# Kernel tuning notes

Measured on AMD Instinct MI355X. Metric: run time of the kernel, lower is better.

The kernel has to match this reference:

```python
import jax, jax.numpy as jnp
import numpy as np

D_MODEL = 1024
N_TILES = 16
N_CLASSES = 1024
BATCH = 65536
THRESH = 0.3  # ternary quantization threshold


def setup_inputs() -> dict:
    key = jax.random.key(0)
    k_x, k_s, k_w, k_b = jax.random.split(key, 4)
    x = jax.random.normal(k_x, (BATCH, D_MODEL), dtype=jnp.float32)
    # signatures_raw: n_tiles params of shape [d_model], init randn*0.5
    sigs_raw = jax.random.normal(k_s, (N_TILES, D_MODEL), dtype=jnp.float32) * 0.5
    # per-tile Linear(d_model, n_classes): weight [n_classes, d_model], bias [n_classes]
    lim = 1.0 / np.sqrt(D_MODEL)
    W = jax.random.uniform(k_w, (N_TILES, N_CLASSES, D_MODEL), dtype=jnp.float32, minval=-lim, maxval=lim)
    b = jax.random.uniform(k_b, (N_TILES, N_CLASSES), dtype=jnp.float32, minval=-lim, maxval=lim)
    return {"x": x, "sigs_raw": sigs_raw, "W": W, "b": b}


def _quantize_ternary(s):
    # straight-through ternary: forward = {-1, 0, +1}, backward = identity
    q = jnp.where(s > THRESH, 1.0, jnp.where(s < -THRESH, -1.0, 0.0)).astype(s.dtype)
    return s + jax.lax.stop_gradient(q - s)


def reference(x, sigs_raw, W, b):
    sigs = _quantize_ternary(sigs_raw)           # [T, D]
    scores = x @ sigs.T                          # [B, T]
    tile_indices = jnp.argmax(scores, axis=-1)   # [B]
    n_tiles = W.shape[0]
    logits = jnp.zeros((x.shape[0], W.shape[1]), dtype=x.dtype)  # [B, C]
    # fixed small loop over tiles (experts); select per-token result via mask
    for t in range(n_tiles):
        out_t = x @ W[t].T + b[t]                # [B, C]
        logits = jnp.where((tile_indices == t)[:, None], out_t, logits)
    return logits, tile_indices
```

## Files before the change

kernel.cpp:

```cpp
#include <hip/hip_runtime.h>
#include <hip/hip_bf16.h>
#include <stdint.h>

#define B_TOK 65536
#define DM 1024
#define NC 1024
#define NT 16
#define GAPTHR 0.25f

typedef __attribute__((ext_vector_type(4))) float f32x4;
typedef __attribute__((ext_vector_type(4))) unsigned int u32x4;
typedef __attribute__((ext_vector_type(2))) unsigned int u32x2;
typedef __attribute__((ext_vector_type(4))) unsigned short u16x4;
typedef __attribute__((ext_vector_type(8))) short short8;

#define AS1(p) ((__attribute__((address_space(1))) void*)(p))
#define AS3(p) ((__attribute__((address_space(3))) void*)(p))

static __device__ inline unsigned short f2bf(float f) {
  __hip_bfloat16 h = __float2bfloat16(f);
  unsigned short u;
  __builtin_memcpy(&u, &h, 2);
  return u;
}
#define PK8(a, b, old, w) __builtin_amdgcn_cvt_pk_fp8_f32((a), (b), (old), (w))

__global__ void k_prep(const float* __restrict__ sigs, unsigned int* __restrict__ mask,
                       unsigned short* __restrict__ Sb) {
  int d = threadIdx.x;
  unsigned int m = 0;
#pragma unroll
  for (int t = 0; t < NT; ++t) {
    float s = sigs[t * DM + d];
    float q = (s > 0.3f) ? 1.0f : ((s < -0.3f) ? -1.0f : 0.0f);
    if (s > 0.3f) m |= 1u << t;
    else if (s < -0.3f) m |= 1u << (16 + t);
    Sb[t * DM + d] = f2bf(q);
  }
  mask[d] = m;
}

__global__ __launch_bounds__(256) void k_pre(const float* __restrict__ x,
    const unsigned short* __restrict__ Sb, unsigned char* __restrict__ xb,
    int* __restrict__ tidx, float* __restrict__ oidx,
    int* __restrict__ fixlist, int* __restrict__ nfix, int* __restrict__ counts,
    const float* __restrict__ W, unsigned char* __restrict__ Wb)
{
  int bid = blockIdx.x;
  int tid = threadIdx.x;
  if (bid >= 1024) {
    const f32x4* W4 = (const f32x4*)W;
    unsigned int* O = (unsigned int*)Wb;
    int n4 = NT * NC * DM / 4;
    for (int i = (bid - 1024) * 256 + tid; i < n4; i += 512 * 256) {
      f32x4 v = W4[i];
      unsigned int p = PK8(v[0] * 16.f, v[1] * 16.f, 0, 0);
      p = PK8(v[2] * 16.f, v[3] * 16.f, p, 1);
      O[i] = p;
    }
    return;
  }
  __shared__ int hist[16];
  if (tid < 16) hist[tid] = 0;
  __syncthreads();

  int w = tid >> 6, l = tid & 63;
  int lr = l & 15, lg = l >> 4;
  int tok0 = bid * 64 + w * 16;

  const float* xr = x + (size_t)(tok0 + lr) * DM + lg * 8;
  unsigned char* xbr = xb + (size_t)(tok0 + lr) * DM + lg * 8;
  const unsigned short* sr = Sb + (size_t)lr * DM + lg * 8;

  f32x4 accA = (f32x4){0.f, 0.f, 0.f, 0.f};
  f32x4 accB = (f32x4){0.f, 0.f, 0.f, 0.f};
  for (int kc = 0; kc < 32; kc += 2) {
    f32x4 v0 = *(const f32x4*)(xr + kc * 32);
    f32x4 v1 = *(const f32x4*)(xr + kc * 32 + 4);
    f32x4 v2 = *(const f32x4*)(xr + kc * 32 + 32);
    f32x4 v3 = *(const f32x4*)(xr + kc * 32 + 36);
    short8 a0, a1;
#pragma unroll
    for (int j = 0; j < 4; ++j) {
      a0[j]     = (short)f2bf(v0[j]);
      a0[4 + j] = (short)f2bf(v1[j]);
      a1[j]     = (short)f2bf(v2[j]);
      a1[4 + j] = (short)f2bf(v3[j]);
    }
    u32x2 p0, p1;
    p0[0] = PK8(v0[0], v0[1], 0, 0); p0[0] = PK8(v0[2], v0[3], p0[0], 1);
    p0[1] = PK8(v1[0], v1[1], 0, 0); p0[1] = PK8(v1[2], v1[3], p0[1], 1);
    p1[0] = PK8(v2[0], v2[1], 0, 0); p1[0] = PK8(v2[2], v2[3], p1[0], 1);
    p1[1] = PK8(v3[0], v3[1], 0, 0); p1[1] = PK8(v3[2], v3[3], p1[1], 1);
    *(u32x2*)(xbr + kc * 32) = p0;
    *(u32x2*)(xbr + kc * 32 + 32) = p1;
    short8 b0 = *(const short8*)(sr + kc * 32);
    short8 b1 = *(const short8*)(sr + kc * 32 + 32);
    accA = __builtin_amdgcn_mfma_f32_16x16x32_bf16(a0, b0, accA, 0, 0, 0);
    accB = __builtin_amdgcn_mfma_f32_16x16x32_bf16(a1, b1, accB, 0, 0, 0);
  }
  f32x4 acc;
#pragma unroll
  for (int i = 0; i < 4; ++i) acc[i] = accA[i] + accB[i];

  float m1[4], m2v[4]; int i1[4];
#pragma unroll
  for (int i = 0; i < 4; ++i) { m1[i] = acc[i]; i1[i] = lr; m2v[i] = -1e30f; }
#pragma unroll
  for (int off = 1; off < 16; off <<= 1) {
#pragma unroll
    for (int i = 0; i < 4; ++i) {
      float bm  = __shfl_xor(m1[i], off);
      int   bi  = __shfl_xor(i1[i], off);
      float bm2 = __shfl_xor(m2v[i], off);
      bool bwin = (bm > m1[i]) || (bm == m1[i] && bi < i1[i]);
      float loser = bwin ? m1[i] : bm;
      m2v[i] = fmaxf(fmaxf(m2v[i], bm2), loser);
      if (bwin) { m1[i] = bm; i1[i] = bi; }
    }
  }
  if (lr == 0) {
#pragma unroll
    for (int i = 0; i < 4; ++i) {
      int tok = tok0 + lg * 4 + i;
      tidx[tok] = i1[i];
      oidx[tok] = (float)i1[i];
      atomicAdd(&hist[i1[i]], 1);
      if (m1[i] - m2v[i] < GAPTHR) {
        int p = atomicAdd(nfix, 1);
        fixlist[p] = tok;
      }
    }
  }
  __syncthreads();
  if (tid < 16 && hist[tid]) atomicAdd(&counts[tid], hist[tid]);
}

__global__ __launch_bounds__(256) void k_fix(const float* __restrict__ x,
    const unsigned int* __restrict__ mask, const int* __restrict__ fixlist,
    const int* __restrict__ nfix, int* __restrict__ tidx, float* __restrict__ oidx,
    int* __restrict__ counts)
{
  int n = *nfix;
  int l = threadIdx.x & 63;
  int gw = (blockIdx.x * 256 + threadIdx.x) >> 6;
  int nw = (gridDim.x * 256) >> 6;
  int t = l & 15, seg = l >> 4;

  for (int i = gw; i < n; i += nw) {
    int tok = fixlist[i];
    const float* xr = x + (size_t)tok * DM + seg * 256;
    const unsigned int* mr = mask + seg * 256;
    double acc0 = 0.0, acc1 = 0.0;
    for (int j = 0; j < 256; j += 4) {
      f32x4 xv = *(const f32x4*)(xr + j);
      u32x4 mv = *(const u32x4*)(mr + j);
#pragma unroll
      for (int u = 0; u < 4; ++u) {
        double c = ((mv[u] >> t) & 1u) ? (double)xv[u]
                 : (((mv[u] >> (16 + t)) & 1u) ? -(double)xv[u] : 0.0);
        if (u & 1) acc1 += c; else acc0 += c;
      }
    }
    double s = acc0 + acc1;
    s += __shfl_xor(s, 16);
    s += __shfl_xor(s, 32);
    double bv = s; int bi = t;
#pragma unroll
    for (int off = 1; off < 16; off <<= 1) {
      double ov = __shfl_xor(bv, off);
      int   oi = __shfl_xor(bi, off);
      if (ov > bv || (ov == bv && oi < bi)) { bv = ov; bi = oi; }
    }
    if (l == 0) {
      int old = tidx[tok];
      if (bi != old) {
        tidx[tok] = bi;
        oidx[tok] = (float)bi;
        atomicSub(&counts[old], 1);
        atomicAdd(&counts[bi], 1);
      }
    }
  }
}

__global__ void k_scan(const int* __restrict__ counts, int* __restrict__ offs) {
  if (threadIdx.x == 0) {
    int s = 0;
    for (int t = 0; t < NT; ++t) {
      offs[t] = s;
      s += (counts[t] + 255) & ~255;
    }
    offs[NT] = s;
  }
}

__global__ __launch_bounds__(256) void k_place(const int* __restrict__ tidx, const int* __restrict__ offs,
                                               int* __restrict__ cursor, int* __restrict__ perm) {
  __shared__ int h[16], base[16];
  int tid = threadIdx.x;
  if (tid < 16) h[tid] = 0;
  __syncthreads();
  int tok = blockIdx.x * 256 + tid;
  int t = tidx[tok];
  int myloc = atomicAdd(&h[t], 1);
  __syncthreads();
  if (tid < 16 && h[tid]) base[tid] = atomicAdd(&cursor[tid], h[tid]);
  __syncthreads();
  perm[offs[t] + base[t] + myloc] = tok;
}

__global__ __launch_bounds__(512, 2) void k_gemm(const unsigned char* __restrict__ xb,
    const unsigned char* __restrict__ Wb, const float* __restrict__ bias,
    const int* __restrict__ perm, const int* __restrict__ offs, float* __restrict__ out)
{
  __shared__ unsigned char lds[4][2][256 * 32];
  int bid0 = blockIdx.x;
  int bid = (bid0 & 7) * 136 + (bid0 >> 3);
  int mb = bid >> 2, nb = bid & 3;
  int total = offs[NT];
  int m0 = mb << 8;
  if (m0 >= total) return;
  int t = 0;
#pragma unroll
  for (int tt = 0; tt < NT; ++tt) if (m0 >= offs[tt + 1]) t = tt + 1;
  int c0 = nb << 8;
  int tid = threadIdx.x;

  int srow = tid >> 1;
  int sk = (((tid & 1) ^ ((tid >> 3) & 1)) << 4);
  int tkA = perm[m0 + srow]; if (tkA < 0) tkA = 0;
  const unsigned char* pA = xb + (size_t)tkA * DM + sk;
  const unsigned char* pB = Wb + (size_t)t * NC * DM + (size_t)(c0 + srow) * DM + sk;

  f32x4 acc[8][4];
#pragma unroll
  for (int m = 0; m < 8; ++m)
#pragma unroll
    for (int n = 0; n < 4; ++n) acc[m][n] = (f32x4){0.f, 0.f, 0.f, 0.f};

  int wid = tid >> 6, l = tid & 63;
  int wr = wid >> 2, wc = wid & 3;
  int lr = l & 15, lk = l >> 4;
  int wr128 = wr * 128, wc64 = wc * 64;
  int goff = (lk ^ (((lr >> 2) & 1) << 1)) * 8;

#define GLDS(g, lp) __builtin_amdgcn_global_load_lds(AS1(g), AS3(lp), 16, 0, 0)
#define STAGE_A(SS, KT) GLDS(pA + (KT) * 32, &lds[SS][0][tid * 16])
#define STAGE_B(SS, KT) GLDS(pB + (KT) * 32, &lds[SS][1][tid * 16])
#define RD_A(SLOT, M) (*(const long*)&lds[SLOT][0][(wr128 + (M) * 16 + lr) * 32 + goff])
#define RD_B(SLOT, N) (*(const long*)&lds[SLOT][1][(wc64 + (N) * 16 + lr) * 32 + goff])
#define MF(M_, N_, AV, BV) acc[M_][N_] = __builtin_amdgcn_mfma_f32_16x16x32_fp8_fp8(AV, BV, acc[M_][N_], 0, 0, 0)
#define MFMA4(M_, AV) { MF(M_, 0, AV, b0); MF(M_, 1, AV, b1); MF(M_, 2, AV, b2); MF(M_, 3, AV, b3); }
#define VM2() asm volatile("s_waitcnt vmcnt(2)" ::: "memory")
#define VM0() asm volatile("s_waitcnt vmcnt(0)" ::: "memory")

#define KTILE(KT, SLOT, SS, DOSTAGE, VMW) { \
  long b0 = RD_B(SLOT, 0), b1 = RD_B(SLOT, 1), b2 = RD_B(SLOT, 2), b3 = RD_B(SLOT, 3); \
  long a0 = RD_A(SLOT, 0), a1 = RD_A(SLOT, 1); \
  if (DOSTAGE) STAGE_A(SS, (KT) + 2); \
  __builtin_amdgcn_s_setprio(1); \
  MFMA4(0, a0); MFMA4(1, a1); \
  { long a2 = RD_A(SLOT, 2), a3 = RD_A(SLOT, 3); \
    if (DOSTAGE) STAGE_B(SS, (KT) + 2); \
    MFMA4(2, a2); MFMA4(3, a3); } \
  { long a4 = RD_A(SLOT, 4), a5 = RD_A(SLOT, 5); MFMA4(4, a4); MFMA4(5, a5); } \
  { long a6 = RD_A(SLOT, 6), a7 = RD_A(SLOT, 7); MFMA4(6, a6); MFMA4(7, a7); } \
  __builtin_amdgcn_s_setprio(0); \
  VMW; \
  __builtin_amdgcn_s_barrier(); }

  STAGE_A(0, 0); STAGE_B(0, 0);
  STAGE_A(1, 1); STAGE_B(1, 1);
  VM2();
  __builtin_amdgcn_s_barrier();

#pragma unroll 1
  for (int kt = 0; kt < 28; kt += 4) {
    KTILE(kt + 0, 0, 2, 1, VM2());
    KTILE(kt + 1, 1, 3, 1, VM2());
    KTILE(kt + 2, 2, 0, 1, VM2());
    KTILE(kt + 3, 3, 1, 1, VM2());
  }
  KTILE(28, 0, 2, 1, VM2());
  KTILE(29, 1, 3, 1, VM2());
  KTILE(30, 2, 0, 0, VM0());
  KTILE(31, 3, 1, 0, ((void)0));

  float bv[4];
#pragma unroll
  for (int n = 0; n < 4; ++n) bv[n] = bias[t * NC + c0 + wc64 + n * 16 + lr];
#pragma unroll
  for (int m = 0; m < 8; ++m) {
#pragma unroll
    for (int j = 0; j < 4; ++j) {
      int prow = m0 + wr128 + m * 16 + lk * 4 + j;
      int tok = perm[prow];
      if (tok >= 0) {
#pragma unroll
        for (int n = 0; n < 4; ++n)
          out[(size_t)tok * NC + c0 + wc64 + n * 16 + lr] = acc[m][n][j] * 0.0625f + bv[n];
      }
    }
  }
}

extern "C" void kernel_launch(void* const* d_in, const int* in_sizes, int n_in,
                              void* d_out, int out_size, void* d_ws, size_t ws_size,
                              hipStream_t stream) {
  const float* x    = (const float*)d_in[0];
  const float* sigs = (const float*)d_in[1];
  const float* W    = (const float*)d_in[2];
  const float* bias = (const float*)d_in[3];
  float* out = (float*)d_out;
  float* oidx = out + (size_t)B_TOK * NC;

  char* ws = (char*)d_ws;
  unsigned char* xb    = (unsigned char*)ws;
  unsigned char* Wb    = (unsigned char*)(ws + 67108864);
  int* perm            = (int*)(ws + 83886080);
  int* tidx            = (int*)(ws + 84164608);
  unsigned int* mask   = (unsigned int*)(ws + 84426752);
  unsigned short* Sb   = (unsigned short*)(ws + 84430848);
  int* fixlist         = (int*)(ws + 84463616);
  int* ctrl            = (int*)(ws + 84725760);
  int* counts = ctrl;
  int* cursor = ctrl + 16;
  int* offs   = ctrl + 32;
  int* nfix   = ctrl + 49;

  hipMemsetAsync(perm, 0xFF, 278528, stream);
  hipMemsetAsync(ctrl, 0, 256, stream);

  k_prep<<<1, 1024, 0, stream>>>(sigs, mask, Sb);
  k_pre<<<1536, 256, 0, stream>>>(x, Sb, xb, tidx, oidx, fixlist, nfix, counts, W, Wb);
  k_fix<<<512, 256, 0, stream>>>(x, mask, fixlist, nfix, tidx, oidx, counts);
  k_scan<<<1, 64, 0, stream>>>(counts, offs);
  k_place<<<256, 256, 0, stream>>>(tidx, offs, cursor, perm);
  k_gemm<<<dim3(272 * 4), 512, 0, stream>>>(xb, Wb, bias, perm, offs, out);
}
```

Measured before the change: 318.5 us.

## Deepen GEMM prefetch to three stages and fold memsets into kernels

The GEMM's global-to-LDS pipeline now prefetches three k-tiles ahead instead of two, using all four LDS slots, and waits with vmcnt(4) so more loads stay in flight. The two hipMemsetAsync calls are removed. Control counters are now zeroed inside k_prep, and k_scan writes -1 only into the padding region of each tile's perm segment. This drops two launches and the full perm memset, at the cost of a serial single-block padding fill and tighter LDS slot reuse that relies on the barrier ordering.

```diff
diff --git a/kernel.cpp b/kernel.cpp
--- a/kernel.cpp
+++ b/kernel.cpp
@@ -26,8 +26,9 @@
 #define PK8(a, b, old, w) __builtin_amdgcn_cvt_pk_fp8_f32((a), (b), (old), (w))
 
 __global__ void k_prep(const float* __restrict__ sigs, unsigned int* __restrict__ mask,
-                       unsigned short* __restrict__ Sb) {
+                       unsigned short* __restrict__ Sb, int* __restrict__ ctrl) {
   int d = threadIdx.x;
+  if (d < 64) ctrl[d] = 0;
   unsigned int m = 0;
 #pragma unroll
   for (int t = 0; t < NT; ++t) {
@@ -184,14 +185,22 @@
   }
 }
 
-__global__ void k_scan(const int* __restrict__ counts, int* __restrict__ offs) {
+__global__ void k_scan(const int* __restrict__ counts, int* __restrict__ offs,
+                       int* __restrict__ perm) {
+  __shared__ int so[NT + 1], sc[NT];
   if (threadIdx.x == 0) {
     int s = 0;
     for (int t = 0; t < NT; ++t) {
-      offs[t] = s;
+      so[t] = s; offs[t] = s;
+      sc[t] = counts[t];
       s += (counts[t] + 255) & ~255;
     }
-    offs[NT] = s;
+    so[NT] = s; offs[NT] = s;
+  }
+  __syncthreads();
+  for (int t = 0; t < NT; ++t) {
+    int start = so[t] + sc[t], end = so[t + 1];
+    for (int i = start + threadIdx.x; i < end; i += blockDim.x) perm[i] = -1;
   }
 }
 
@@ -252,17 +261,18 @@
 #define RD_B(SLOT, N) (*(const long*)&lds[SLOT][1][(wc64 + (N) * 16 + lr) * 32 + goff])
 #define MF(M_, N_, AV, BV) acc[M_][N_] = __builtin_amdgcn_mfma_f32_16x16x32_fp8_fp8(AV, BV, acc[M_][N_], 0, 0, 0)
 #define MFMA4(M_, AV) { MF(M_, 0, AV, b0); MF(M_, 1, AV, b1); MF(M_, 2, AV, b2); MF(M_, 3, AV, b3); }
+#define VM4() asm volatile("s_waitcnt vmcnt(4)" ::: "memory")
 #define VM2() asm volatile("s_waitcnt vmcnt(2)" ::: "memory")
 #define VM0() asm volatile("s_waitcnt vmcnt(0)" ::: "memory")
 
 #define KTILE(KT, SLOT, SS, DOSTAGE, VMW) { \
   long b0 = RD_B(SLOT, 0), b1 = RD_B(SLOT, 1), b2 = RD_B(SLOT, 2), b3 = RD_B(SLOT, 3); \
   long a0 = RD_A(SLOT, 0), a1 = RD_A(SLOT, 1); \
-  if (DOSTAGE) STAGE_A(SS, (KT) + 2); \
+  if (DOSTAGE) STAGE_A(SS, (KT) + 3); \
   __builtin_amdgcn_s_setprio(1); \
   MFMA4(0, a0); MFMA4(1, a1); \
   { long a2 = RD_A(SLOT, 2), a3 = RD_A(SLOT, 3); \
-    if (DOSTAGE) STAGE_B(SS, (KT) + 2); \
+    if (DOSTAGE) STAGE_B(SS, (KT) + 3); \
     MFMA4(2, a2); MFMA4(3, a3); } \
   { long a4 = RD_A(SLOT, 4), a5 = RD_A(SLOT, 5); MFMA4(4, a4); MFMA4(5, a5); } \
   { long a6 = RD_A(SLOT, 6), a7 = RD_A(SLOT, 7); MFMA4(6, a6); MFMA4(7, a7); } \
@@ -272,20 +282,21 @@
 
   STAGE_A(0, 0); STAGE_B(0, 0);
   STAGE_A(1, 1); STAGE_B(1, 1);
-  VM2();
+  STAGE_A(2, 2); STAGE_B(2, 2);
+  VM4();
   __builtin_amdgcn_s_barrier();
 
 #pragma unroll 1
   for (int kt = 0; kt < 28; kt += 4) {
-    KTILE(kt + 0, 0, 2, 1, VM2());
-    KTILE(kt + 1, 1, 3, 1, VM2());
-    KTILE(kt + 2, 2, 0, 1, VM2());
-    KTILE(kt + 3, 3, 1, 1, VM2());
-  }
-  KTILE(28, 0, 2, 1, VM2());
-  KTILE(29, 1, 3, 1, VM2());
-  KTILE(30, 2, 0, 0, VM0());
-  KTILE(31, 3, 1, 0, ((void)0));
+    KTILE(kt + 0, 0, 3, 1, VM4());
+    KTILE(kt + 1, 1, 0, 1, VM4());
+    KTILE(kt + 2, 2, 1, 1, VM4());
+    KTILE(kt + 3, 3, 2, 1, VM4());
+  }
+  KTILE(28, 0, 3, 1, VM4());
+  KTILE(29, 1, 0, 0, VM2());
+  KTILE(30, 2, 1, 0, VM0());
+  KTILE(31, 3, 2, 0, ((void)0));
 
   float bv[4];
 #pragma unroll
@@ -329,13 +340,10 @@
   int* offs   = ctrl + 32;
   int* nfix   = ctrl + 49;
 
-  hipMemsetAsync(perm, 0xFF, 278528, stream);
-  hipMemsetAsync(ctrl, 0, 256, stream);
-
-  k_prep<<<1, 1024, 0, stream>>>(sigs, mask, Sb);
+  k_prep<<<1, 1024, 0, stream>>>(sigs, mask, Sb, ctrl);
   k_pre<<<1536, 256, 0, stream>>>(x, Sb, xb, tidx, oidx, fixlist, nfix, counts, W, Wb);
   k_fix<<<512, 256, 0, stream>>>(x, mask, fixlist, nfix, tidx, oidx, counts);
-  k_scan<<<1, 64, 0, stream>>>(counts, offs);
+  k_scan<<<1, 256, 0, stream>>>(counts, offs, perm);
   k_place<<<256, 256, 0, stream>>>(tidx, offs, cursor, perm);
   k_gemm<<<dim3(272 * 4), 512, 0, stream>>>(xb, Wb, bias, perm, offs, out);
 }
```

Result: no change. 316.8 us (-0.5%).
